# Kernel tuning notes

Measured on AMD Instinct MI355X. Metric: run time of the kernel, lower is better.

## Reference

```python
import jax, jax.numpy as jnp
import numpy as np

B, T, D = 4, 2048, 1024
H = 16
HD = D // H  # 64

def setup_inputs() -> dict:
    key = jax.random.key(0)
    k1, k2, k3 = jax.random.split(key, 3)
    x = jax.random.normal(k1, (B, T, D), dtype=jnp.float32)
    # torch nn.Linear weight layout: [out_features, in_features]
    w_qkv = jax.random.normal(k2, (3 * D, D), dtype=jnp.float32) * (D ** -0.5)
    w_proj = jax.random.normal(k3, (D, D), dtype=jnp.float32) * (D ** -0.5)
    return {"x": x, "w_qkv": w_qkv, "w_proj": w_proj}

def reference(x, w_qkv, w_proj):
    b, t, c = x.shape
    qkv = jnp.einsum('btc,oc->bto', x, w_qkv)  # [b,t,3c]
    q, k, v = jnp.split(qkv, 3, axis=-1)
    # [b,h,t,hd]
    q = q.reshape(b, t, H, HD).transpose(0, 2, 1, 3)
    k = k.reshape(b, t, H, HD).transpose(0, 2, 1, 3)
    v = v.reshape(b, t, H, HD).transpose(0, 2, 1, 3)
    att = jnp.einsum('bhqd,bhkd->bhqk', q, k) / (HD ** 0.5)
    causal = jnp.tril(jnp.ones((t, t), dtype=bool))
    att = jnp.where(causal, att, -jnp.inf)
    att = jax.nn.softmax(att, axis=-1)
    y = jnp.einsum('bhqk,bhkd->bhqd', att, v)
    y = y.transpose(0, 2, 1, 3).reshape(b, t, c)
    return jnp.einsum('btc,oc->bto', y, w_proj)
```

## Files before the change

### kernel.cpp

```cpp
#include <hip/hip_runtime.h>
#include <cstdint>
#include <cstddef>


typedef __bf16 bf16;
typedef __bf16 bf16x4 __attribute__((ext_vector_type(4)));
typedef __bf16 bf16x8 __attribute__((ext_vector_type(8)));
typedef float  f32x4  __attribute__((ext_vector_type(4)));
typedef float  fvec4  __attribute__((ext_vector_type(4)));
typedef unsigned u32x2 __attribute__((ext_vector_type(2)));

typedef __attribute__((address_space(1))) const void global_cv;
typedef __attribute__((address_space(3))) void lds_v;

#define MFMA16(a, b, c) __builtin_amdgcn_mfma_f32_16x16x32_bf16((a), (b), (c), 0, 0, 0)

#define QSCALE 0.18033688f

__device__ __forceinline__ void async_ld16(const bf16* g, bf16* l) {
  __builtin_amdgcn_global_load_lds((global_cv*)g, (lds_v*)l, 16, 0, 0);
}

__device__ __forceinline__ int swz_off(int row, int col) {
  int sr = (row & 7) ^ ((row >> 3) & 7);
  return row * 64 + ((((col >> 3) ^ sr) & 7) * 8) + (col & 7);
}

__device__ __forceinline__ unsigned cvt_pk(float lo, float hi) {
  unsigned r;
  asm("v_cvt_pk_bf16_f32 %0, %1, %2" : "=v"(r) : "v"(lo), "v"(hi));
  return r;
}

__device__ __forceinline__ float exp2_fast(float x) {
  float r;
  asm("v_exp_f32 %0, %1" : "=v"(r) : "v"(x));
  return r;
}

__device__ __forceinline__ bf16x8 cvt8(const float* p) {
  fvec4 u = *(const fvec4*)p;
  fvec4 v = *(const fvec4*)(p + 4);
  bf16x8 r;
  r[0] = (bf16)u[0]; r[1] = (bf16)u[1]; r[2] = (bf16)u[2]; r[3] = (bf16)u[3];
  r[4] = (bf16)v[0]; r[5] = (bf16)v[1]; r[6] = (bf16)v[2]; r[7] = (bf16)v[3];
  return r;
}

__global__ void cvt_all(const float* __restrict__ x, const float* __restrict__ wq,
                        const float* __restrict__ wp, bf16* __restrict__ xb,
                        bf16* __restrict__ wqb, bf16* __restrict__ wpb) {
  int i = blockIdx.x * 256 + threadIdx.x;
  const float* s;
  bf16* d;
  int off;
  if (i < 1048576)      { s = x;  d = xb;  off = i; }
  else if (i < 1441792) { s = wq; d = wqb; off = i - 1048576; }
  else                  { s = wp; d = wpb; off = i - 1441792; }
  *(bf16x8*)(d + (size_t)off * 8) = cvt8(s + (size_t)off * 8);
}

__device__ __forceinline__ void qkv_scatter(const f32x4 acc[4][4], int m0, int n0,
                                            int wm, int wn, int quad, int l15,
                                            bf16* Qo, bf16* Ko, bf16* Vo) {
  const int which = n0 >> 10;
  if (which == 2) {
#pragma unroll
    for (int i = 0; i < 4; ++i) {
      const int m = m0 + wm + i * 16 + quad * 4;
      const int b = m >> 11;
      const int t = m & 2047;
#pragma unroll
      for (int j = 0; j < 4; ++j) {
        const int n1 = (n0 + wn + j * 16 + l15) & 1023;
        const int h  = n1 >> 6;
        const int d  = n1 & 63;
        bf16x4 v;
#pragma unroll
        for (int r = 0; r < 4; ++r) v[r] = (bf16)acc[i][j][r];
        *(bf16x4*)(Vo + ((size_t)(b * 16 + h) * 64 + d) * 2048 + t) = v;
      }
    }
    return;
  }
  bf16* dst = (which == 0) ? Qo : Ko;
  const float scale = (which == 0) ? QSCALE : 1.0f;
#pragma unroll
  for (int i = 0; i < 4; ++i) {
    const int m = m0 + wm + i * 16 + quad * 4;
#pragma unroll
    for (int j = 0; j < 4; ++j) {
      const int n  = n0 + wn + j * 16 + l15;
      const int n1 = n & 1023;
      const int h  = n1 >> 6;
      const int d  = n1 & 63;
#pragma unroll
      for (int r = 0; r < 4; ++r) {
        const int mm = m + r;
        const int b  = mm >> 11;
        const int t  = mm & 2047;
        dst[(((size_t)(b * 16 + h)) * 2048 + t) * 64 + d] =
            (bf16)(acc[i][j][r] * scale);
      }
    }
  }
}

__global__ __launch_bounds__(256, 3)
void gemm_qkv_a(const bf16* __restrict__ A, const bf16* __restrict__ B,
                bf16* __restrict__ Qo, bf16* __restrict__ Ko,
                bf16* __restrict__ Vo) {
  __shared__ __align__(16) bf16 As[2 * 128 * 32];
  __shared__ __align__(16) bf16 Bs[2 * 128 * 32];
  const int K = 1024;

  const int tid  = threadIdx.x;
  const int lane = tid & 63;
  const int wave = tid >> 6;
  const int quad = lane >> 4;
  const int l15  = lane & 15;
  const int wm   = (wave >> 1) * 64;
  const int wn   = (wave & 1) * 64;

  const int lin = (int)blockIdx.x + (int)blockIdx.y * 24;
  const int xcd = lin & 7;
  const int sl  = lin >> 3;
  const int n0  = (xcd * 3 + (sl % 3)) * 128;
  const int m0  = (sl / 3) * 128;

  f32x4 acc[4][4];
#pragma unroll
  for (int i = 0; i < 4; ++i)
#pragma unroll
    for (int j = 0; j < 4; ++j) acc[i][j] = f32x4{0.f, 0.f, 0.f, 0.f};

  const int r0 = tid >> 2;
  const int c0 = (tid & 3) * 8;
  const bf16* ag0 = A + (size_t)(m0 + r0) * K + c0;
  const bf16* ag1 = A + (size_t)(m0 + 64 + r0) * K + c0;
  const bf16* bg0 = B + (size_t)(n0 + r0) * K + c0;
  const bf16* bg1 = B + (size_t)(n0 + 64 + r0) * K + c0;
  const int lo0 = (wave * 64) * 8;
  const int lo1 = (256 + wave * 64) * 8;

  const int afb = (wm + l15) * 64 + quad * 16;
  const int bfb = (wn + l15) * 64 + quad * 16;

  async_ld16(ag0, As + lo0);
  async_ld16(ag1, As + lo1);
  async_ld16(bg0, Bs + lo0);
  async_ld16(bg1, Bs + lo1);
  ag0 += 32; ag1 += 32; bg0 += 32; bg1 += 32;
  __syncthreads();

  for (int it = 0; it < 32; ++it) {
    const int cur = it & 1;
    if (it < 31) {
      const int nb = (cur ^ 1) << 12;
      async_ld16(ag0, As + nb + lo0);
      async_ld16(ag1, As + nb + lo1);
      async_ld16(bg0, Bs + nb + lo0);
      async_ld16(bg1, Bs + nb + lo1);
      ag0 += 32; ag1 += 32; bg0 += 32; bg1 += 32;
    }

    const char* pA = (const char*)As + (cur << 13) + afb;
    const char* pB = (const char*)Bs + (cur << 13) + bfb;
    bf16x8 af[4], bfr[4];
#pragma unroll
    for (int i = 0; i < 4; ++i) af[i] = *(const bf16x8*)(pA + i * 1024);
#pragma unroll
    for (int j = 0; j < 4; ++j) bfr[j] = *(const bf16x8*)(pB + j * 1024);
#pragma unroll
    for (int i = 0; i < 4; ++i)
#pragma unroll
      for (int j = 0; j < 4; ++j)
        acc[i][j] = MFMA16(af[i], bfr[j], acc[i][j]);

    __syncthreads();
  }
  qkv_scatter(acc, m0, n0, wm, wn, quad, l15, Qo, Ko, Vo);
}

__global__ __launch_bounds__(256, 2)
void gemm_qkv_f(const float* __restrict__ A, const float* __restrict__ B,
                bf16* __restrict__ Qo, bf16* __restrict__ Ko,
                bf16* __restrict__ Vo) {
  __shared__ __align__(16) bf16 As[128 * 32];
  __shared__ __align__(16) bf16 Bs[128 * 32];
  const int K = 1024;

  const int tid  = threadIdx.x;
  const int lane = tid & 63;
  const int wave = tid >> 6;
  const int quad = lane >> 4;
  const int l15  = lane & 15;
  const int wm   = (wave >> 1) * 64;
  const int wn   = (wave & 1) * 64;

  const int lin = (int)blockIdx.x + (int)blockIdx.y * 24;
  const int xcd = lin & 7;
  const int sl  = lin >> 3;
  const int n0  = (xcd * 3 + (sl % 3)) * 128;
  const int m0  = (sl / 3) * 128;

  f32x4 acc[4][4];
#pragma unroll
  for (int i = 0; i < 4; ++i)
#pragma unroll
    for (int j = 0; j < 4; ++j) acc[i][j] = f32x4{0.f, 0.f, 0.f, 0.f};

  const int r0 = tid >> 2;
  const int c0 = (tid & 3) * 8;
  const size_t aoff0 = (size_t)(m0 + r0) * K + c0;
  const size_t aoff1 = (size_t)(m0 + 64 + r0) * K + c0;
  const size_t boff0 = (size_t)(n0 + r0) * K + c0;
  const size_t boff1 = (size_t)(n0 + 64 + r0) * K + c0;

  for (int k0 = 0; k0 < K; k0 += 32) {
    bf16x8 va0 = cvt8(A + aoff0 + k0);
    bf16x8 va1 = cvt8(A + aoff1 + k0);
    bf16x8 vb0 = cvt8(B + boff0 + k0);
    bf16x8 vb1 = cvt8(B + boff1 + k0);
    __syncthreads();
    *(bf16x8*)(As + tid * 8)        = va0;
    *(bf16x8*)(As + 2048 + tid * 8) = va1;
    *(bf16x8*)(Bs + tid * 8)        = vb0;
    *(bf16x8*)(Bs + 2048 + tid * 8) = vb1;
    __syncthreads();

    bf16x8 af[4], bfr[4];
#pragma unroll
    for (int i = 0; i < 4; ++i)
      af[i] = *(const bf16x8*)(As + (wm + i * 16 + l15) * 32 + quad * 8);
#pragma unroll
    for (int j = 0; j < 4; ++j)
      bfr[j] = *(const bf16x8*)(Bs + (wn + j * 16 + l15) * 32 + quad * 8);
#pragma unroll
    for (int i = 0; i < 4; ++i)
#pragma unroll
      for (int j = 0; j < 4; ++j)
        acc[i][j] = MFMA16(af[i], bfr[j], acc[i][j]);
  }
  qkv_scatter(acc, m0, n0, wm, wn, quad, l15, Qo, Ko, Vo);
}

__global__ __launch_bounds__(256, 3)
void attn(const bf16* __restrict__ Q, const bf16* __restrict__ Kk,
          const bf16* __restrict__ Vt, bf16* __restrict__ Y) {
  __shared__ __align__(16) bf16 Ks[2][64 * 64];
  __shared__ __align__(16) bf16 Vs[2][64 * 64];
  __shared__ __align__(16) bf16 Ps[4 * 16 * 64];

  const int tid  = threadIdx.x;
  const int wave = tid >> 6;
  const int lane = tid & 63;
  const int quad = lane >> 4;
  const int l15  = lane & 15;

  const int lin  = (int)blockIdx.x + ((int)blockIdx.y << 4);
  const int slot = lin >> 3;
  const int bh   = (lin & 7) * 8 + (slot >> 4);
  const int p    = slot & 15;
  const int b    = bh >> 4;
  const int h    = bh & 15;

  const bf16* Qb = Q  + (size_t)bh * (2048 * 64);
  const bf16* Kb = Kk + (size_t)bh * (2048 * 64);
  const bf16* Vb = Vt + (size_t)bh * (2048 * 64);
  char* Pw = (char*)(Ps + wave * (16 * 64));

  const int r0s = wave * 8 + (lane >> 3);
  const int r1s = r0s + 32;
  const int qch = lane & 7;
  const int co0 = (((qch ^ ((r0s & 7) ^ ((r0s >> 3) & 7)))) & 7) * 8;
  const int co1 = (((qch ^ ((r1s & 7) ^ ((r1s >> 3) & 7)))) & 7) * 8;
  const bf16* kg0 = Kb + (size_t)r0s * 64 + co0;
  const bf16* kg1 = Kb + (size_t)r1s * 64 + co1;
  const bf16* vg0 = Vb + (size_t)r0s * 2048 + co0;
  const bf16* vg1 = Vb + (size_t)r1s * 2048 + co1;
  const int ldsw = wave * 512;

  const int psx   = l15 & 7;
  const int prowb = l15 * 128;
  const int pr0   = prowb + ((quad ^ psx) << 4);
  const int pr1   = prowb + (((4 + quad) ^ psx) << 4);

  int fo0[4], fo1[4];
#pragma unroll
  for (int j = 0; j < 4; ++j) {
    const int kvr = j * 16 + l15;
    fo0[j] = swz_off(kvr, quad * 8) * 2;
    fo1[j] = swz_off(kvr, 32 + quad * 8) * 2;
  }
  int pwo[4];
#pragma unroll
  for (int j = 0; j < 4; ++j)
    pwo[j] = prowb + ((((2 * j + (quad >> 1)) ^ psx) << 4) | ((quad & 1) << 3));

  const float NEG = -1e30f;

#pragma unroll 1
  for (int pass = 0; pass < 2; ++pass) {
    const int qt = pass ? (31 - p) : p;
    const int q0 = qt * 64;

    const bf16* qp = Qb + (size_t)(q0 + wave * 16 + l15) * 64 + quad * 8;
    bf16x8 qa0 = *(const bf16x8*)qp;
    bf16x8 qa1 = *(const bf16x8*)(qp + 32);

    f32x4 l4 = {0.f, 0.f, 0.f, 0.f};
    f32x4 o[4];
#pragma unroll
    for (int j = 0; j < 4; ++j) o[j] = f32x4{0.f, 0.f, 0.f, 0.f};

    async_ld16(kg0, Ks[0] + ldsw);
    async_ld16(kg1, Ks[0] + 2048 + ldsw);
    async_ld16(vg0, Vs[0] + ldsw);
    async_ld16(vg1, Vs[0] + 2048 + ldsw);
    __syncthreads();

#pragma unroll 1
    for (int kt = 0; kt <= qt; ++kt) {
      const int cur = kt & 1;
      const int k0  = kt * 64;

      if (kt < qt) {
        const int kn = k0 + 64;
        async_ld16(kg0 + (size_t)kn * 64, Ks[cur ^ 1] + ldsw);
        async_ld16(kg1 + (size_t)kn * 64, Ks[cur ^ 1] + 2048 + ldsw);
        async_ld16(vg0 + kn, Vs[cur ^ 1] + ldsw);
        async_ld16(vg1 + kn, Vs[cur ^ 1] + 2048 + ldsw);
      }

      const char* kc = (const char*)Ks[cur];

      f32x4 s[4];
      __builtin_amdgcn_s_setprio(1);
#pragma unroll
      for (int j = 0; j < 4; ++j) {
        bf16x8 k0f = *(const bf16x8*)(kc + fo0[j]);
        bf16x8 k1f = *(const bf16x8*)(kc + fo1[j]);
        f32x4 z = {0.f, 0.f, 0.f, 0.f};
        z = MFMA16(k0f, qa0, z);
        z = MFMA16(k1f, qa1, z);
        s[j] = z;
      }
      __builtin_amdgcn_s_setprio(0);

      if (kt == qt) {
        const int qloc = wave * 16 + l15;
#pragma unroll
        for (int j = 0; j < 4; ++j) {
#pragma unroll
          for (int r = 0; r < 4; ++r) {
            if (16 * j + 4 * quad + r > qloc) s[j][r] = NEG;
          }
        }
      }

#pragma unroll
      for (int j = 0; j < 4; ++j) {
#pragma unroll
        for (int r = 0; r < 4; ++r) s[j][r] = exp2_fast(s[j][r]);
        l4 += s[j];
      }

#pragma unroll
      for (int j = 0; j < 4; ++j) {
        u32x2 pk;
        pk[0] = cvt_pk(s[j][0], s[j][1]);
        pk[1] = cvt_pk(s[j][2], s[j][3]);
        *(u32x2*)(Pw + pwo[j]) = pk;
      }

      bf16x8 pf0 = *(const bf16x8*)(Pw + pr0);
      bf16x8 pf1 = *(const bf16x8*)(Pw + pr1);

      const char* vc = (const char*)Vs[cur];
      __builtin_amdgcn_s_setprio(1);
#pragma unroll
      for (int j = 0; j < 4; ++j) {
        bf16x8 vf0 = *(const bf16x8*)(vc + fo0[j]);
        bf16x8 vf1 = *(const bf16x8*)(vc + fo1[j]);
        o[j] = MFMA16(pf0, vf0, o[j]);
        o[j] = MFMA16(pf1, vf1, o[j]);
      }
      __builtin_amdgcn_s_setprio(0);

      __syncthreads();
    }

    float lf = (l4[0] + l4[1]) + (l4[2] + l4[3]);
    lf += __shfl_xor(lf, 16);
    lf += __shfl_xor(lf, 32);
    float inv[4];
#pragma unroll
    for (int r = 0; r < 4; ++r) inv[r] = 1.0f / __shfl(lf, quad * 4 + r);

#pragma unroll
    for (int j = 0; j < 4; ++j) {
      const int dcol = h * 64 + j * 16 + l15;
#pragma unroll
      for (int r = 0; r < 4; ++r) {
        const int trow = q0 + wave * 16 + quad * 4 + r;
        Y[((size_t)b * 2048 + trow) * 1024 + dcol] = (bf16)(o[j][r] * inv[r]);
      }
    }
  }
}

__global__ __launch_bounds__(256, 3)
void gemm_proj_a(const bf16* __restrict__ A, const bf16* __restrict__ B,
                 float* __restrict__ C) {
  __shared__ __align__(16) bf16 As[2 * 128 * 32];
  __shared__ __align__(16) bf16 Bs[2 * 128 * 32];
  const int K = 1024, N = 1024;

  const int tid  = threadIdx.x;
  const int lane = tid & 63;
  const int wave = tid >> 6;
  const int quad = lane >> 4;
  const int l15  = lane & 15;
  const int wm   = (wave >> 1) * 64;
  const int wn   = (wave & 1) * 64;

  const int lin = (int)blockIdx.x + (int)blockIdx.y * 8;
  const int xcd = lin & 7;
  const int sl  = lin >> 3;
  const int m0  = (xcd * 8 + (sl & 7)) * 128;
  const int n0  = (sl >> 3) * 128;

  f32x4 acc[4][4];
#pragma unroll
  for (int i = 0; i < 4; ++i)
#pragma unroll
    for (int j = 0; j < 4; ++j) acc[i][j] = f32x4{0.f, 0.f, 0.f, 0.f};

  const int r0 = tid >> 2;
  const int c0 = (tid & 3) * 8;
  const bf16* ag0 = A + (size_t)(m0 + r0) * K + c0;
  const bf16* ag1 = A + (size_t)(m0 + 64 + r0) * K + c0;
  const bf16* bg0 = B + (size_t)(n0 + r0) * K + c0;
  const bf16* bg1 = B + (size_t)(n0 + 64 + r0) * K + c0;
  const int lo0 = (wave * 64) * 8;
  const int lo1 = (256 + wave * 64) * 8;

  const int afb = (wm + l15) * 64 + quad * 16;
  const int bfb = (wn + l15) * 64 + quad * 16;

  async_ld16(ag0, As + lo0);
  async_ld16(ag1, As + lo1);
  async_ld16(bg0, Bs + lo0);
  async_ld16(bg1, Bs + lo1);
  ag0 += 32; ag1 += 32; bg0 += 32; bg1 += 32;
  __syncthreads();

  for (int it = 0; it < 32; ++it) {
    const int cur = it & 1;
    if (it < 31) {
      const int nb = (cur ^ 1) << 12;
      async_ld16(ag0, As + nb + lo0);
      async_ld16(ag1, As + nb + lo1);
      async_ld16(bg0, Bs + nb + lo0);
      async_ld16(bg1, Bs + nb + lo1);
      ag0 += 32; ag1 += 32; bg0 += 32; bg1 += 32;
    }

    const char* pA = (const char*)As + (cur << 13) + afb;
    const char* pB = (const char*)Bs + (cur << 13) + bfb;
    bf16x8 af[4], bfr[4];
#pragma unroll
    for (int i = 0; i < 4; ++i) af[i] = *(const bf16x8*)(pA + i * 1024);
#pragma unroll
    for (int j = 0; j < 4; ++j) bfr[j] = *(const bf16x8*)(pB + j * 1024);
#pragma unroll
    for (int i = 0; i < 4; ++i)
#pragma unroll
      for (int j = 0; j < 4; ++j)
        acc[i][j] = MFMA16(af[i], bfr[j], acc[i][j]);

    __syncthreads();
  }

#pragma unroll
  for (int i = 0; i < 4; ++i) {
    const int m = m0 + wm + i * 16 + quad * 4;
#pragma unroll
    for (int j = 0; j < 4; ++j) {
      const int n = n0 + wn + j * 16 + l15;
#pragma unroll
      for (int r = 0; r < 4; ++r)
        C[(size_t)(m + r) * N + n] = acc[i][j][r];
    }
  }
}

__global__ __launch_bounds__(256, 2)
void gemm_proj_f(const bf16* __restrict__ A, const float* __restrict__ B,
                 float* __restrict__ C) {
  __shared__ __align__(16) bf16 As[128 * 32];
  __shared__ __align__(16) bf16 Bs[128 * 32];
  const int K = 1024, N = 1024;

  const int tid  = threadIdx.x;
  const int lane = tid & 63;
  const int wave = tid >> 6;
  const int quad = lane >> 4;
  const int l15  = lane & 15;
  const int wm   = (wave >> 1) * 64;
  const int wn   = (wave & 1) * 64;

  const int lin = (int)blockIdx.x + (int)blockIdx.y * 8;
  const int xcd = lin & 7;
  const int sl  = lin >> 3;
  const int m0  = (xcd * 8 + (sl & 7)) * 128;
  const int n0  = (sl >> 3) * 128;

  f32x4 acc[4][4];
#pragma unroll
  for (int i = 0; i < 4; ++i)
#pragma unroll
    for (int j = 0; j < 4; ++j) acc[i][j] = f32x4{0.f, 0.f, 0.f, 0.f};

  const int r0 = tid >> 2;
  const int c0 = (tid & 3) * 8;
  const size_t aoff0 = (size_t)(m0 + r0) * K + c0;
  const size_t aoff1 = (size_t)(m0 + 64 + r0) * K + c0;
  const size_t boff0 = (size_t)(n0 + r0) * K + c0;
  const size_t boff1 = (size_t)(n0 + 64 + r0) * K + c0;

  for (int k0 = 0; k0 < K; k0 += 32) {
    bf16x8 va0 = *(const bf16x8*)(A + aoff0 + k0);
    bf16x8 va1 = *(const bf16x8*)(A + aoff1 + k0);
    bf16x8 vb0 = cvt8(B + boff0 + k0);
    bf16x8 vb1 = cvt8(B + boff1 + k0);
    __syncthreads();
    *(bf16x8*)(As + tid * 8)        = va0;
    *(bf16x8*)(As + 2048 + tid * 8) = va1;
    *(bf16x8*)(Bs + tid * 8)        = vb0;
    *(bf16x8*)(Bs + 2048 + tid * 8) = vb1;
    __syncthreads();

    bf16x8 af[4], bfr[4];
#pragma unroll
    for (int i = 0; i < 4; ++i)
      af[i] = *(const bf16x8*)(As + (wm + i * 16 + l15) * 32 + quad * 8);
#pragma unroll
    for (int j = 0; j < 4; ++j)
      bfr[j] = *(const bf16x8*)(Bs + (wn + j * 16 + l15) * 32 + quad * 8);
#pragma unroll
    for (int i = 0; i < 4; ++i)
#pragma unroll
      for (int j = 0; j < 4; ++j)
        acc[i][j] = MFMA16(af[i], bfr[j], acc[i][j]);
  }

#pragma unroll
  for (int i = 0; i < 4; ++i) {
    const int m = m0 + wm + i * 16 + quad * 4;
#pragma unroll
    for (int j = 0; j < 4; ++j) {
      const int n = n0 + wn + j * 16 + l15;
#pragma unroll
      for (int r = 0; r < 4; ++r)
        C[(size_t)(m + r) * N + n] = acc[i][j][r];
    }
  }
}

extern "C" void kernel_launch(void* const* d_in, const int* in_sizes, int n_in,
                              void* d_out, int out_size, void* d_ws, size_t ws_size,
                              hipStream_t stream) {
  const float* x  = nullptr;
  const float* wq = nullptr;
  const float* wp = nullptr;
  for (int i = 0; i < n_in; ++i) {
    if      (in_sizes[i] == 8388608) x  = (const float*)d_in[i];
    else if (in_sizes[i] == 3145728) wq = (const float*)d_in[i];
    else if (in_sizes[i] == 1048576) wp = (const float*)d_in[i];
  }
  if (!x || !wq || !wp) {
    x = (const float*)d_in[0]; wq = (const float*)d_in[1]; wp = (const float*)d_in[2];
  }

  float* out = (float*)d_out;
  const size_t NE = (size_t)4 * 16 * 2048 * 64;
  bf16* kb = (bf16*)d_ws;
  bf16* vb = kb + NE;
  bf16* qb = vb + NE;
  bf16* yb = qb + NE;
  bf16* xb  = yb + NE;
  bf16* wqb = xb + 8388608;
  bf16* wpb = wqb + 3145728;
  const size_t need = (4 * NE + 8388608 + 3145728 + 1048576) * sizeof(bf16);
  const bool ext = ws_size >= need;

  if (ext) {
    cvt_all<<<6144, 256, 0, stream>>>(x, wq, wp, xb, wqb, wpb);
    gemm_qkv_a<<<dim3(24, 64), 256, 0, stream>>>(xb, wqb, qb, kb, vb);
  } else {
    gemm_qkv_f<<<dim3(24, 64), 256, 0, stream>>>(x, wq, qb, kb, vb);
  }

  attn<<<dim3(16, 64), 256, 0, stream>>>(qb, kb, vb, yb);

  if (ext) {
    gemm_proj_a<<<dim3(8, 64), 256, 0, stream>>>(yb, wpb, out);
  } else {
    gemm_proj_f<<<dim3(8, 64), 256, 0, stream>>>(yb, wp, out);
  }
}
```

Measured before the change: 241.0 us.

## Triple-buffer LDS in bf16 QKV and projection GEMMs with partial vmcnt waits

Both bf16 GEMM kernels move from double- to triple-buffered LDS staging. Two tiles are prefetched up front, and each iteration waits only until the older tile has landed (vmcnt(4)) instead of doing a full __syncthreads. This keeps two async global-to-LDS loads in flight during MFMA work to hide memory latency. In exchange, LDS per block grows to 48KB, which may limit the three-blocks-per-CU occupancy target, and the hand-written waitcnt logic is fragile.

```diff
diff --git a/kernel.cpp b/kernel.cpp
--- a/kernel.cpp
+++ b/kernel.cpp
@@ -110,8 +110,8 @@
 void gemm_qkv_a(const bf16* __restrict__ A, const bf16* __restrict__ B,
                 bf16* __restrict__ Qo, bf16* __restrict__ Ko,
                 bf16* __restrict__ Vo) {
-  __shared__ __align__(16) bf16 As[2 * 128 * 32];
-  __shared__ __align__(16) bf16 Bs[2 * 128 * 32];
+  __shared__ __align__(16) bf16 As[3 * 128 * 32];
+  __shared__ __align__(16) bf16 Bs[3 * 128 * 32];
   const int K = 1024;
 
   const int tid  = threadIdx.x;
@@ -151,21 +151,28 @@
   async_ld16(bg0, Bs + lo0);
   async_ld16(bg1, Bs + lo1);
   ag0 += 32; ag1 += 32; bg0 += 32; bg1 += 32;
-  __syncthreads();
-
+  async_ld16(ag0, As + 4096 + lo0);
+  async_ld16(ag1, As + 4096 + lo1);
+  async_ld16(bg0, Bs + 4096 + lo0);
+  async_ld16(bg1, Bs + 4096 + lo1);
+  ag0 += 32; ag1 += 32; bg0 += 32; bg1 += 32;
+  asm volatile("s_waitcnt vmcnt(4)" ::: "memory");
+  __builtin_amdgcn_s_barrier();
+  __builtin_amdgcn_sched_barrier(0);
+
+  int cure = 0;
+  int nxte = 8192;
   for (int it = 0; it < 32; ++it) {
-    const int cur = it & 1;
-    if (it < 31) {
-      const int nb = (cur ^ 1) << 12;
-      async_ld16(ag0, As + nb + lo0);
-      async_ld16(ag1, As + nb + lo1);
-      async_ld16(bg0, Bs + nb + lo0);
-      async_ld16(bg1, Bs + nb + lo1);
+    if (it < 30) {
+      async_ld16(ag0, As + nxte + lo0);
+      async_ld16(ag1, As + nxte + lo1);
+      async_ld16(bg0, Bs + nxte + lo0);
+      async_ld16(bg1, Bs + nxte + lo1);
       ag0 += 32; ag1 += 32; bg0 += 32; bg1 += 32;
     }
 
-    const char* pA = (const char*)As + (cur << 13) + afb;
-    const char* pB = (const char*)Bs + (cur << 13) + bfb;
+    const char* pA = (const char*)As + cure * 2 + afb;
+    const char* pB = (const char*)Bs + cure * 2 + bfb;
     bf16x8 af[4], bfr[4];
 #pragma unroll
     for (int i = 0; i < 4; ++i) af[i] = *(const bf16x8*)(pA + i * 1024);
@@ -177,7 +184,13 @@
       for (int j = 0; j < 4; ++j)
         acc[i][j] = MFMA16(af[i], bfr[j], acc[i][j]);
 
-    __syncthreads();
+    if (it < 30) asm volatile("s_waitcnt vmcnt(4)" ::: "memory");
+    else         asm volatile("s_waitcnt vmcnt(0)" ::: "memory");
+    __builtin_amdgcn_s_barrier();
+    __builtin_amdgcn_sched_barrier(0);
+
+    cure = (cure == 8192) ? 0 : cure + 4096;
+    nxte = (nxte == 8192) ? 0 : nxte + 4096;
   }
   qkv_scatter(acc, m0, n0, wm, wn, quad, l15, Qo, Ko, Vo);
 }
@@ -413,8 +426,8 @@
 __global__ __launch_bounds__(256, 3)
 void gemm_proj_a(const bf16* __restrict__ A, const bf16* __restrict__ B,
                  float* __restrict__ C) {
-  __shared__ __align__(16) bf16 As[2 * 128 * 32];
-  __shared__ __align__(16) bf16 Bs[2 * 128 * 32];
+  __shared__ __align__(16) bf16 As[3 * 128 * 32];
+  __shared__ __align__(16) bf16 Bs[3 * 128 * 32];
   const int K = 1024, N = 1024;
 
   const int tid  = threadIdx.x;
@@ -454,21 +467,28 @@
   async_ld16(bg0, Bs + lo0);
   async_ld16(bg1, Bs + lo1);
   ag0 += 32; ag1 += 32; bg0 += 32; bg1 += 32;
-  __syncthreads();
-
+  async_ld16(ag0, As + 4096 + lo0);
+  async_ld16(ag1, As + 4096 + lo1);
+  async_ld16(bg0, Bs + 4096 + lo0);
+  async_ld16(bg1, Bs + 4096 + lo1);
+  ag0 += 32; ag1 += 32; bg0 += 32; bg1 += 32;
+  asm volatile("s_waitcnt vmcnt(4)" ::: "memory");
+  __builtin_amdgcn_s_barrier();
+  __builtin_amdgcn_sched_barrier(0);
+
+  int cure = 0;
+  int nxte = 8192;
   for (int it = 0; it < 32; ++it) {
-    const int cur = it & 1;
-    if (it < 31) {
-      const int nb = (cur ^ 1) << 12;
-      async_ld16(ag0, As + nb + lo0);
-      async_ld16(ag1, As + nb + lo1);
-      async_ld16(bg0, Bs + nb + lo0);
-      async_ld16(bg1, Bs + nb + lo1);
+    if (it < 30) {
+      async_ld16(ag0, As + nxte + lo0);
+      async_ld16(ag1, As + nxte + lo1);
+      async_ld16(bg0, Bs + nxte + lo0);
+      async_ld16(bg1, Bs + nxte + lo1);
       ag0 += 32; ag1 += 32; bg0 += 32; bg1 += 32;
     }
 
-    const char* pA = (const char*)As + (cur << 13) + afb;
-    const char* pB = (const char*)Bs + (cur << 13) + bfb;
+    const char* pA = (const char*)As + cure * 2 + afb;
+    const char* pB = (const char*)Bs + cure * 2 + bfb;
     bf16x8 af[4], bfr[4];
 #pragma unroll
     for (int i = 0; i < 4; ++i) af[i] = *(const bf16x8*)(pA + i * 1024);
@@ -480,7 +500,13 @@
       for (int j = 0; j < 4; ++j)
         acc[i][j] = MFMA16(af[i], bfr[j], acc[i][j]);
 
-    __syncthreads();
+    if (it < 30) asm volatile("s_waitcnt vmcnt(4)" ::: "memory");
+    else         asm volatile("s_waitcnt vmcnt(0)" ::: "memory");
+    __builtin_amdgcn_s_barrier();
+    __builtin_amdgcn_sched_barrier(0);
+
+    cure = (cure == 8192) ? 0 : cure + 4096;
+    nxte = (nxte == 8192) ? 0 : nxte + 4096;
   }
 
 #pragma unroll
```

Result: no change. 241.6 us (+0.3%).
